# Kernel optimization log

Hardware: AMD Instinct MI355X
Metric: run time of the kernel (lower is better)

The kernel has to match this reference:

```python
import jax, jax.numpy as jnp
import numpy as np

B, N, D, H = 4, 2048, 512, 8
HD = D // H  # head_dim = 64
EPS = 1e-5


def setup_inputs() -> dict:
    key = jax.random.key(0)
    ks = jax.random.split(key, 12)
    x = jax.random.normal(ks[0], (B, N, D), dtype=jnp.float32)
    adj = jax.random.randint(ks[1], (B, N, N), 0, 2, dtype=jnp.int32)
    # self-loops so no softmax row is fully masked
    adj = jnp.maximum(adj, jnp.eye(N, dtype=jnp.int32)[None, :, :])
    s = 1.0 / np.sqrt(D)
    Wq = jax.random.uniform(ks[2], (D, D), jnp.float32, -s, s)
    bq = jnp.zeros((D,), jnp.float32)
    Wk = jax.random.uniform(ks[3], (D, D), jnp.float32, -s, s)
    bk = jnp.zeros((D,), jnp.float32)
    Wv = jax.random.uniform(ks[4], (D, D), jnp.float32, -s, s)
    bv = jnp.zeros((D,), jnp.float32)
    Wo = jax.random.uniform(ks[5], (D, D), jnp.float32, -s, s)
    bo = jnp.zeros((D,), jnp.float32)
    gamma = jnp.ones((D,), jnp.float32)
    beta = jnp.zeros((D,), jnp.float32)
    return {"x": x, "adj": adj, "Wq": Wq, "bq": bq, "Wk": Wk, "bk": bk,
            "Wv": Wv, "bv": bv, "Wo": Wo, "bo": bo, "gamma": gamma, "beta": beta}


def reference(x, adj, Wq, bq, Wk, bk, Wv, bv, Wo, bo, gamma, beta):
    b, n, d = x.shape
    scale = 1.0 / np.sqrt(HD).astype(np.float32)
    # QKV projections -> (b, n, H, HD)
    q = (x @ Wq + bq).reshape(b, n, H, HD)
    k = (x @ Wk + bk).reshape(b, n, H, HD)
    v = (x @ Wv + bv).reshape(b, n, H, HD)
    # scores: (b, H, n, n)
    scores = jnp.einsum('bnhd,bmhd->bhnm', q, k) * scale
    mask = (adj == 0)[:, None, :, :]  # (b, 1, n, n)
    scores = jnp.where(mask, jnp.float32(-jnp.inf), scores)
    attn = jax.nn.softmax(scores, axis=-1)
    h = jnp.einsum('bhnm,bmhd->bnhd', attn, v).reshape(b, n, d)
    h = h @ Wo + bo
    # residual + LayerNorm
    y = h + x
    mu = jnp.mean(y, axis=-1, keepdims=True)
    var = jnp.mean(jnp.square(y - mu), axis=-1, keepdims=True)
    return (y - mu) * jax.lax.rsqrt(var + EPS) * gamma + beta
```

## Files before the change

### kernel.cpp

```cpp
#include <hip/hip_runtime.h>
#include <hip/hip_bf16.h>

#define Bsz 4
#define Nn 2048
#define Dd 512
#define Hh 8
#define HDim 64
#define MTOT (Bsz * Nn)

typedef unsigned short ush;
typedef __bf16 bf16x8 __attribute__((ext_vector_type(8)));
typedef float f32x4 __attribute__((ext_vector_type(4)));

__device__ __forceinline__ ush f2bf(float f) {
    unsigned u = __builtin_bit_cast(unsigned, f);
    unsigned r = (u + 0x7fffu + ((u >> 16) & 1u)) >> 16;
    return (ush)r;
}
__device__ __forceinline__ unsigned cvtpk(float a, float b) {
    unsigned r;
    asm("v_cvt_pk_bf16_f32 %0, %1, %2" : "=v"(r) : "v"(a), "v"(b));
    return r;
}

#define GLOAD_LDS(g, l)                                                       \
    __builtin_amdgcn_global_load_lds(                                         \
        (const __attribute__((address_space(1))) unsigned int*)(g),           \
        (__attribute__((address_space(3))) unsigned int*)(l), 16, 0, 0)

__global__ __launch_bounds__(256) void convert_bf16(const float* __restrict__ src,
                                                    ush* __restrict__ dst, int n) {
    int i = (blockIdx.x * 256 + threadIdx.x) * 4;
    if (i < n) {
        float4 v = *reinterpret_cast<const float4*>(src + i);
        dst[i + 0] = f2bf(v.x);
        dst[i + 1] = f2bf(v.y);
        dst[i + 2] = f2bf(v.z);
        dst[i + 3] = f2bf(v.w);
    }
}

__global__ __launch_bounds__(256) void transpose_bf16(const float* __restrict__ src,
                                                      ush* __restrict__ dst) {
    __shared__ ush tile[64][72];
    const int k0 = blockIdx.x * 64, n0 = blockIdx.y * 64;
    const int t = threadIdx.x;
    const int r = t >> 2, c = (t & 3) * 16;
#pragma unroll
    for (int i = 0; i < 4; ++i) {
        float4 v = *reinterpret_cast<const float4*>(src + (size_t)(k0 + r) * Dd + n0 + c + i * 4);
        tile[r][c + i * 4 + 0] = f2bf(v.x);
        tile[r][c + i * 4 + 1] = f2bf(v.y);
        tile[r][c + i * 4 + 2] = f2bf(v.z);
        tile[r][c + i * 4 + 3] = f2bf(v.w);
    }
    __syncthreads();
    const int rn = t >> 2, kc = (t & 3) * 16;
    ush ov[16];
#pragma unroll
    for (int j = 0; j < 16; ++j) ov[j] = tile[kc + j][rn];
    *reinterpret_cast<uint4*>(dst + (size_t)(n0 + rn) * Dd + k0 + kc) =
        *reinterpret_cast<uint4*>(&ov[0]);
    *reinterpret_cast<uint4*>(dst + (size_t)(n0 + rn) * Dd + k0 + kc + 8) =
        *reinterpret_cast<uint4*>(&ov[8]);
}

__global__ __launch_bounds__(256) void adj_to_bits(const int* __restrict__ adj,
                                                   unsigned* __restrict__ bits) {
    int idx = blockIdx.x * 256 + threadIdx.x;
    const int* p = adj + (size_t)(idx >> 6) * Nn + (idx & 63) * 32;
    unsigned m = 0;
#pragma unroll
    for (int v4 = 0; v4 < 8; ++v4) {
        int4 v = *reinterpret_cast<const int4*>(p + v4 * 4);
        if (v.x) m |= 1u << (v4 * 4 + 0);
        if (v.y) m |= 1u << (v4 * 4 + 1);
        if (v.z) m |= 1u << (v4 * 4 + 2);
        if (v.w) m |= 1u << (v4 * 4 + 3);
    }
    bits[idx] = m;
}

__global__ __launch_bounds__(256) void gemm_bf16(const ush* __restrict__ A,
                                                 const ush* __restrict__ Wt,
                                                 const float* __restrict__ bias,
                                                 int mode, ush* __restrict__ outb,
                                                 float* __restrict__ outf) {
    __shared__ __align__(16) ush As[2][128][32];
    __shared__ __align__(16) ush Bs[2][64][32];
    const int t = threadIdx.x, lane = t & 63, w = t >> 6;
    const int ln = lane & 15, gr = lane >> 4;
    const int m0 = blockIdx.x * 128, n0 = blockIdx.y * 64;
    const int wm = w >> 1, wn = w & 1;

    f32x4 acc[4][2] = {};

    const int arow_in_op = lane >> 2;
    const int achk = (lane & 3) * 8;

#define STAGE_A(buf, k0)                                                          \
    {                                                                             \
        _Pragma("unroll") for (int o = 0; o < 2; ++o) {                           \
            int r0 = o * 64 + w * 16;                                             \
            int rr = r0 + arow_in_op;                                             \
            GLOAD_LDS(A + (size_t)(m0 + rr) * Dd + (k0) + achk, &As[buf][r0][0]); \
        }                                                                         \
    }
#define STAGE_B(buf, k0)                                                          \
    {                                                                             \
        int r0 = w * 16;                                                          \
        int rr = r0 + arow_in_op;                                                 \
        GLOAD_LDS(Wt + (size_t)(n0 + rr) * Dd + (k0) + achk, &Bs[buf][r0][0]);    \
    }

    STAGE_A(0, 0);
    STAGE_B(0, 0);
    __syncthreads();

    for (int it = 0; it < 16; ++it) {
        const int buf = it & 1;
        if (it < 15) {
            STAGE_A(buf ^ 1, (it + 1) * 32);
            STAGE_B(buf ^ 1, (it + 1) * 32);
        }
        bf16x8 af[4], bfr[2];
#pragma unroll
        for (int i = 0; i < 4; ++i)
            af[i] = *reinterpret_cast<const bf16x8*>(&As[buf][wm * 64 + i * 16 + ln][gr * 8]);
#pragma unroll
        for (int j = 0; j < 2; ++j)
            bfr[j] = *reinterpret_cast<const bf16x8*>(&Bs[buf][wn * 32 + j * 16 + ln][gr * 8]);
#pragma unroll
        for (int i = 0; i < 4; ++i)
#pragma unroll
            for (int j = 0; j < 2; ++j)
                acc[i][j] = __builtin_amdgcn_mfma_f32_16x16x32_bf16(af[i], bfr[j], acc[i][j], 0, 0, 0);
        __syncthreads();
    }

#pragma unroll
    for (int i = 0; i < 4; ++i) {
#pragma unroll
        for (int j = 0; j < 2; ++j) {
#pragma unroll
            for (int r = 0; r < 4; ++r) {
                int row = m0 + wm * 64 + i * 16 + gr * 4 + r;
                int col = n0 + wn * 32 + j * 16 + ln;
                float v = acc[i][j][r] + bias[col];
                if (mode == 2) {
                    outf[(size_t)row * Dd + col] = v;
                } else {
                    int b = row >> 11, n = row & (Nn - 1);
                    int h = col >> 6, hd = col & 63;
                    if (mode == 0)
                        outb[(((size_t)(b * Hh + h)) * Nn + n) * HDim + hd] = f2bf(v);
                    else
                        outb[(((size_t)(b * Hh + h)) * HDim + hd) * Nn + n] = f2bf(v);
                }
            }
        }
    }
#undef STAGE_A
#undef STAGE_B
}

__global__ __launch_bounds__(256) void attn_kernel(const ush* __restrict__ Q,
                                                   const ush* __restrict__ K,
                                                   const ush* __restrict__ Vt,
                                                   const unsigned* __restrict__ bits,
                                                   ush* __restrict__ O) {
    __shared__ __align__(16) ush Ktile[2][64][64];
    __shared__ __align__(16) ush Vtile[2][64][64];
    __shared__ __align__(16) ush Pl[4][16][64];
    const int t = threadIdx.x, lane = t & 63, w = t >> 6;
    const int ln = lane & 15, gr = lane >> 4;
    const int blk = blockIdx.x;
    const int qt = blk & 31;
    const int bh = blk >> 5;
    const int b = bh >> 3, h = bh & 7;
    const int q0 = qt * 64 + w * 16;

    const ush* Qb = Q + (size_t)bh * Nn * HDim;
    const ush* Kb = K + (size_t)bh * Nn * HDim;
    const ush* Vb = Vt + (size_t)bh * HDim * Nn;
    const unsigned* rowbits = bits + ((size_t)b * Nn + q0 + ln) * (Nn / 32);

    char* plbase = (char*)&Pl[w][0][0];
    const int lnm = ln & 7;

    const int srow_in_op = lane >> 3;
    const int schk = lane & 7;

#define STAGE_K(buf, kv0)                                                              \
    {                                                                                  \
        _Pragma("unroll") for (int o = 0; o < 2; ++o) {                                \
            int r0 = o * 32 + w * 8;                                                   \
            int rr = r0 + srow_in_op;                                                  \
            int cc = schk ^ (rr & 7);                                                  \
            GLOAD_LDS(Kb + (size_t)((kv0) + rr) * HDim + cc * 8, &Ktile[buf][r0][0]);  \
        }                                                                              \
    }
#define STAGE_V(buf, kv0)                                                              \
    {                                                                                  \
        _Pragma("unroll") for (int o = 0; o < 2; ++o) {                                \
            int r0 = o * 32 + w * 8;                                                   \
            int rr = r0 + srow_in_op;                                                  \
            int cc = schk ^ (rr & 7);                                                  \
            GLOAD_LDS(Vb + (size_t)rr * Nn + (kv0) + cc * 8, &Vtile[buf][r0][0]);      \
        }                                                                              \
    }

    bf16x8 bq0 = *reinterpret_cast<const bf16x8*>(Qb + (size_t)(q0 + ln) * HDim + gr * 8);
    bf16x8 bq1 = *reinterpret_cast<const bf16x8*>(Qb + (size_t)(q0 + ln) * HDim + 32 + gr * 8);

    f32x4 accO[4] = {};
    float mrow = -1e30f, lrow = 0.f;
    const float SCL = 0.125f * 1.44269504f;

    STAGE_K(0, 0);
    STAGE_V(0, 0);
    __syncthreads();

    for (int step = 0; step < 32; ++step) {
        const int kv0 = step * 64;
        const int buf = step & 1;
        if (step < 31) {
            STAGE_K(buf ^ 1, kv0 + 64);
            STAGE_V(buf ^ 1, kv0 + 64);
        }

        unsigned w0 = rowbits[kv0 >> 5];
        unsigned w1 = rowbits[(kv0 >> 5) + 1];

        f32x4 s[4];
#pragma unroll
        for (int kt = 0; kt < 4; ++kt) {
            bf16x8 a0 = *reinterpret_cast<const bf16x8*>(
                &Ktile[buf][kt * 16 + ln][((gr) ^ lnm) * 8]);
            bf16x8 a1 = *reinterpret_cast<const bf16x8*>(
                &Ktile[buf][kt * 16 + ln][((4 + gr) ^ lnm) * 8]);
            f32x4 z = {};
            z = __builtin_amdgcn_mfma_f32_16x16x32_bf16(a0, bq0, z, 0, 0, 0);
            s[kt] = __builtin_amdgcn_mfma_f32_16x16x32_bf16(a1, bq1, z, 0, 0, 0);
        }

        float p[4][4];
        float mk[4];
#pragma unroll
        for (int kt = 0; kt < 4; ++kt) {
            unsigned wsel = (kt >= 2) ? w1 : w0;
#pragma unroll
            for (int r = 0; r < 4; ++r) {
                float sv = s[kt][r] * SCL;
                int bit = (kt * 16 + 4 * gr + r) & 31;
                p[kt][r] = ((wsel >> bit) & 1u) ? sv : -1e30f;
            }
            mk[kt] = fmaxf(fmaxf(p[kt][0], p[kt][1]), fmaxf(p[kt][2], p[kt][3]));
        }
        float mc = fmaxf(fmaxf(mk[0], mk[1]), fmaxf(mk[2], mk[3]));
        mc = fmaxf(mc, __shfl_xor(mc, 16));
        mc = fmaxf(mc, __shfl_xor(mc, 32));
        float mn = fmaxf(mrow, mc);
        float alpha = __builtin_amdgcn_exp2f(mrow - mn);
        mrow = mn;

        float sk[4];
#pragma unroll
        for (int kt = 0; kt < 4; ++kt) {
#pragma unroll
            for (int r = 0; r < 4; ++r) p[kt][r] = __builtin_amdgcn_exp2f(p[kt][r] - mn);
            sk[kt] = (p[kt][0] + p[kt][1]) + (p[kt][2] + p[kt][3]);
        }
        float ps = (sk[0] + sk[1]) + (sk[2] + sk[3]);
        ps += __shfl_xor(ps, 16);
        ps += __shfl_xor(ps, 32);
        lrow = lrow * alpha + ps;
#pragma unroll
        for (int t2 = 0; t2 < 4; ++t2)
#pragma unroll
            for (int r = 0; r < 4; ++r) accO[t2][r] *= alpha;

#pragma unroll
        for (int kt = 0; kt < 4; ++kt) {
            unsigned pk0 = cvtpk(p[kt][0], p[kt][1]);
            unsigned pk1 = cvtpk(p[kt][2], p[kt][3]);
            int blkw = (2 * kt + (gr >> 1)) ^ lnm;
            *reinterpret_cast<uint2*>(plbase + ln * 128 + blkw * 16 + 8 * (gr & 1)) =
                make_uint2(pk0, pk1);
        }
#pragma unroll
        for (int c = 0; c < 2; ++c) {
            bf16x8 pf = *reinterpret_cast<const bf16x8*>(
                plbase + ln * 128 + (((4 * c + gr) ^ lnm) * 16));
#pragma unroll
            for (int t2 = 0; t2 < 4; ++t2) {
                bf16x8 vf = *reinterpret_cast<const bf16x8*>(
                    &Vtile[buf][t2 * 16 + ln][((c * 4 + gr) ^ lnm) * 8]);
                accO[t2] = __builtin_amdgcn_mfma_f32_16x16x32_bf16(vf, pf, accO[t2], 0, 0, 0);
            }
        }
        __syncthreads();
    }

    float inv = 1.0f / lrow;
#pragma unroll
    for (int t2 = 0; t2 < 4; ++t2) {
        unsigned o0 = cvtpk(accO[t2][0] * inv, accO[t2][1] * inv);
        unsigned o1 = cvtpk(accO[t2][2] * inv, accO[t2][3] * inv);
        int blkw = (2 * t2 + (gr >> 1)) ^ lnm;
        *reinterpret_cast<uint2*>(plbase + ln * 128 + blkw * 16 + 8 * (gr & 1)) =
            make_uint2(o0, o1);
    }
    int qr = lane >> 2, cs = lane & 3;
#pragma unroll
    for (int half = 0; half < 2; ++half) {
        int blkr = (cs * 2 + half) ^ (qr & 7);
        uint4 val = *reinterpret_cast<const uint4*>(plbase + qr * 128 + blkr * 16);
        *reinterpret_cast<uint4*>(O + ((size_t)(b * Nn + qt * 64 + w * 16 + qr)) * Dd +
                                  h * 64 + cs * 16 + half * 8) = val;
    }
#undef STAGE_K
#undef STAGE_V
}

__global__ __launch_bounds__(256) void ln_kernel(const float* __restrict__ hbuf,
                                                 const float* __restrict__ x,
                                                 const float* __restrict__ gamma,
                                                 const float* __restrict__ beta,
                                                 float* __restrict__ out) {
    const int row = blockIdx.x;
    const int t = threadIdx.x;
    const float* hr = hbuf + (size_t)row * Dd;
    const float* xr = x + (size_t)row * Dd;
    float y0 = hr[t] + xr[t];
    float y1 = hr[t + 256] + xr[t + 256];

    __shared__ float red[4];
    float s = y0 + y1;
#pragma unroll
    for (int m = 32; m; m >>= 1) s += __shfl_xor(s, m);
    if ((t & 63) == 0) red[t >> 6] = s;
    __syncthreads();
    float mu = (red[0] + red[1] + red[2] + red[3]) * (1.0f / Dd);

    float d0 = y0 - mu, d1 = y1 - mu;
    float vs = d0 * d0 + d1 * d1;
#pragma unroll
    for (int m = 32; m; m >>= 1) vs += __shfl_xor(vs, m);
    __syncthreads();
    if ((t & 63) == 0) red[t >> 6] = vs;
    __syncthreads();
    float var = (red[0] + red[1] + red[2] + red[3]) * (1.0f / Dd);
    float rs = rsqrtf(var + 1e-5f);

    out[(size_t)row * Dd + t] = d0 * rs * gamma[t] + beta[t];
    out[(size_t)row * Dd + t + 256] = d1 * rs * gamma[t + 256] + beta[t + 256];
}

extern "C" void kernel_launch(void* const* d_in, const int* in_sizes, int n_in,
                              void* d_out, int out_size, void* d_ws, size_t ws_size,
                              hipStream_t stream) {
    const float* x = (const float*)d_in[0];
    const int* adj = (const int*)d_in[1];
    const float* Wq = (const float*)d_in[2];
    const float* bq = (const float*)d_in[3];
    const float* Wk = (const float*)d_in[4];
    const float* bk = (const float*)d_in[5];
    const float* Wv = (const float*)d_in[6];
    const float* bv = (const float*)d_in[7];
    const float* Wo = (const float*)d_in[8];
    const float* bo = (const float*)d_in[9];
    const float* gamma = (const float*)d_in[10];
    const float* beta = (const float*)d_in[11];
    float* out = (float*)d_out;

    const size_t MD = (size_t)MTOT * Dd;
    const size_t WW = (size_t)Dd * Dd;
    ush* ws = (ush*)d_ws;
    ush* xb = ws;
    ush* Wqb = xb + MD;
    ush* Wkb = Wqb + WW;
    ush* Wvb = Wkb + WW;
    ush* Wob = Wvb + WW;
    ush* Qb = Wob + WW;
    ush* Kb = Qb + MD;
    ush* Vtb = Kb + MD;
    ush* Ob = Vtb + MD;
    float* hbuf = (float*)(Ob + MD);
    unsigned* bitsbuf = (unsigned*)hbuf;

    convert_bf16<<<dim3((int)(MD / 1024)), dim3(256), 0, stream>>>(x, xb, (int)MD);
    dim3 tg(Dd / 64, Dd / 64), bb(256);
    transpose_bf16<<<tg, bb, 0, stream>>>(Wq, Wqb);
    transpose_bf16<<<tg, bb, 0, stream>>>(Wk, Wkb);
    transpose_bf16<<<tg, bb, 0, stream>>>(Wv, Wvb);
    transpose_bf16<<<tg, bb, 0, stream>>>(Wo, Wob);

    adj_to_bits<<<dim3(MTOT * 64 / 256), dim3(256), 0, stream>>>(adj, bitsbuf);

    dim3 gg(MTOT / 128, Dd / 64);
    gemm_bf16<<<gg, bb, 0, stream>>>(xb, Wqb, bq, 0, Qb, nullptr);
    gemm_bf16<<<gg, bb, 0, stream>>>(xb, Wkb, bk, 0, Kb, nullptr);
    gemm_bf16<<<gg, bb, 0, stream>>>(xb, Wvb, bv, 1, Vtb, nullptr);

    attn_kernel<<<dim3(Bsz * Hh * (Nn / 64)), bb, 0, stream>>>(Qb, Kb, Vtb, bitsbuf, Ob);

    gemm_bf16<<<gg, bb, 0, stream>>>(Ob, Wob, bo, 2, nullptr, hbuf);

    ln_kernel<<<dim3(MTOT), bb, 0, stream>>>(hbuf, x, gamma, beta, out);
}
```

Before: 291.4 us.

## Fuse QKV projections into one 128x128 GEMM, fold scale, lazy softmax rescale

The three QKV projection GEMMs become a single launch over a concatenated transposed weight buffer, and the GEMM tile grows from 128x64 to 128x128 for more reuse per staged load. The softmax scale is folded into the Q projection epilogue, which removes a multiply per score in the attention loop. The attention kernel now skips the running-max update and the accumulator rescale unless the max grows by more than 8 in log2 units, cutting per-step VALU work. The risks are fewer blocks for the output projection, higher register pressure from the larger accumulator, and exp2 values up to 2^8 in bf16 P, which costs some precision headroom.

```diff
diff --git a/kernel.cpp b/kernel.cpp
--- a/kernel.cpp
+++ b/kernel.cpp
@@ -81,87 +81,96 @@
     bits[idx] = m;
 }
 
-__global__ __launch_bounds__(256) void gemm_bf16(const ush* __restrict__ A,
-                                                 const ush* __restrict__ Wt,
-                                                 const float* __restrict__ bias,
-                                                 int mode, ush* __restrict__ outb,
-                                                 float* __restrict__ outf) {
+__global__ __launch_bounds__(256) void gemm128(const ush* __restrict__ A,
+                                               const ush* __restrict__ Wt,
+                                               const float* __restrict__ bq,
+                                               const float* __restrict__ bk,
+                                               const float* __restrict__ bv,
+                                               ush* __restrict__ outQ,
+                                               ush* __restrict__ outK,
+                                               ush* __restrict__ outVt,
+                                               float* __restrict__ outF, int fused) {
     __shared__ __align__(16) ush As[2][128][32];
-    __shared__ __align__(16) ush Bs[2][64][32];
+    __shared__ __align__(16) ush Bs[2][128][32];
     const int t = threadIdx.x, lane = t & 63, w = t >> 6;
     const int ln = lane & 15, gr = lane >> 4;
-    const int m0 = blockIdx.x * 128, n0 = blockIdx.y * 64;
+    const int m0 = blockIdx.x * 128, n0 = blockIdx.y * 128;
     const int wm = w >> 1, wn = w & 1;
 
-    f32x4 acc[4][2] = {};
-
-    const int arow_in_op = lane >> 2;
-    const int achk = (lane & 3) * 8;
-
-#define STAGE_A(buf, k0)                                                          \
-    {                                                                             \
-        _Pragma("unroll") for (int o = 0; o < 2; ++o) {                           \
-            int r0 = o * 64 + w * 16;                                             \
-            int rr = r0 + arow_in_op;                                             \
-            GLOAD_LDS(A + (size_t)(m0 + rr) * Dd + (k0) + achk, &As[buf][r0][0]); \
-        }                                                                         \
-    }
-#define STAGE_B(buf, k0)                                                          \
-    {                                                                             \
-        int r0 = w * 16;                                                          \
-        int rr = r0 + arow_in_op;                                                 \
-        GLOAD_LDS(Wt + (size_t)(n0 + rr) * Dd + (k0) + achk, &Bs[buf][r0][0]);    \
-    }
-
-    STAGE_A(0, 0);
-    STAGE_B(0, 0);
+    f32x4 acc[4][4] = {};
+    const int srow = lane >> 2, schk = (lane & 3) * 8;
+
+#define STG(buf, k0)                                                               \
+    {                                                                              \
+        _Pragma("unroll") for (int o = 0; o < 2; ++o) {                            \
+            int r0 = o * 64 + w * 16;                                              \
+            int rr = r0 + srow;                                                    \
+            GLOAD_LDS(A + (size_t)(m0 + rr) * Dd + (k0) + schk, &As[buf][r0][0]);  \
+            GLOAD_LDS(Wt + (size_t)(n0 + rr) * Dd + (k0) + schk, &Bs[buf][r0][0]); \
+        }                                                                          \
+    }
+
+    STG(0, 0);
     __syncthreads();
 
     for (int it = 0; it < 16; ++it) {
         const int buf = it & 1;
-        if (it < 15) {
-            STAGE_A(buf ^ 1, (it + 1) * 32);
-            STAGE_B(buf ^ 1, (it + 1) * 32);
-        }
-        bf16x8 af[4], bfr[2];
+        if (it < 15) STG(buf ^ 1, (it + 1) * 32);
+        bf16x8 af[4], bf_[4];
 #pragma unroll
         for (int i = 0; i < 4; ++i)
             af[i] = *reinterpret_cast<const bf16x8*>(&As[buf][wm * 64 + i * 16 + ln][gr * 8]);
 #pragma unroll
-        for (int j = 0; j < 2; ++j)
-            bfr[j] = *reinterpret_cast<const bf16x8*>(&Bs[buf][wn * 32 + j * 16 + ln][gr * 8]);
+        for (int j = 0; j < 4; ++j)
+            bf_[j] = *reinterpret_cast<const bf16x8*>(&Bs[buf][wn * 64 + j * 16 + ln][gr * 8]);
 #pragma unroll
         for (int i = 0; i < 4; ++i)
 #pragma unroll
-            for (int j = 0; j < 2; ++j)
-                acc[i][j] = __builtin_amdgcn_mfma_f32_16x16x32_bf16(af[i], bfr[j], acc[i][j], 0, 0, 0);
+            for (int j = 0; j < 4; ++j)
+                acc[i][j] = __builtin_amdgcn_mfma_f32_16x16x32_bf16(af[i], bf_[j], acc[i][j], 0, 0, 0);
         __syncthreads();
     }
 
-#pragma unroll
-    for (int i = 0; i < 4; ++i) {
-#pragma unroll
-        for (int j = 0; j < 2; ++j) {
-#pragma unroll
-            for (int r = 0; r < 4; ++r) {
-                int row = m0 + wm * 64 + i * 16 + gr * 4 + r;
-                int col = n0 + wn * 32 + j * 16 + ln;
-                float v = acc[i][j][r] + bias[col];
-                if (mode == 2) {
-                    outf[(size_t)row * Dd + col] = v;
-                } else {
+    const float SCL = 0.125f * 1.44269504f;
+    if (fused) {
+        const int qkv = blockIdx.y >> 2;
+        const float* bias = (qkv == 0) ? bq : ((qkv == 1) ? bk : bv);
+        const float scale = (qkv == 0) ? SCL : 1.0f;
+#pragma unroll
+        for (int i = 0; i < 4; ++i) {
+#pragma unroll
+            for (int j = 0; j < 4; ++j) {
+#pragma unroll
+                for (int r = 0; r < 4; ++r) {
+                    int row = m0 + wm * 64 + i * 16 + gr * 4 + r;
+                    int colq = (n0 & 511) + wn * 64 + j * 16 + ln;
+                    float v = (acc[i][j][r] + bias[colq]) * scale;
                     int b = row >> 11, n = row & (Nn - 1);
-                    int h = col >> 6, hd = col & 63;
-                    if (mode == 0)
-                        outb[(((size_t)(b * Hh + h)) * Nn + n) * HDim + hd] = f2bf(v);
-                    else
-                        outb[(((size_t)(b * Hh + h)) * HDim + hd) * Nn + n] = f2bf(v);
+                    int h = colq >> 6, hd = colq & 63;
+                    if (qkv == 2)
+                        outVt[(((size_t)(b * Hh + h)) * HDim + hd) * Nn + n] = f2bf(v);
+                    else {
+                        ush* o = (qkv == 0) ? outQ : outK;
+                        o[(((size_t)(b * Hh + h)) * Nn + n) * HDim + hd] = f2bf(v);
+                    }
                 }
             }
         }
-    }
-#undef STAGE_A
-#undef STAGE_B
+    } else {
+#pragma unroll
+        for (int i = 0; i < 4; ++i) {
+#pragma unroll
+            for (int j = 0; j < 4; ++j) {
+#pragma unroll
+                for (int r = 0; r < 4; ++r) {
+                    int row = m0 + wm * 64 + i * 16 + gr * 4 + r;
+                    int col = n0 + wn * 64 + j * 16 + ln;
+                    outF[(size_t)row * Dd + col] = acc[i][j][r] + bq[col];
+                }
+            }
+        }
+    }
+#undef STG
 }
 
 __global__ __launch_bounds__(256) void attn_kernel(const ush* __restrict__ Q,
@@ -215,7 +224,6 @@
 
     f32x4 accO[4] = {};
     float mrow = -1e30f, lrow = 0.f;
-    const float SCL = 0.125f * 1.44269504f;
 
     STAGE_K(0, 0);
     STAGE_V(0, 0);
@@ -251,7 +259,7 @@
             unsigned wsel = (kt >= 2) ? w1 : w0;
 #pragma unroll
             for (int r = 0; r < 4; ++r) {
-                float sv = s[kt][r] * SCL;
+                float sv = s[kt][r];
                 int bit = (kt * 16 + 4 * gr + r) & 31;
                 p[kt][r] = ((wsel >> bit) & 1u) ? sv : -1e30f;
             }
@@ -260,25 +268,29 @@
         float mc = fmaxf(fmaxf(mk[0], mk[1]), fmaxf(mk[2], mk[3]));
         mc = fmaxf(mc, __shfl_xor(mc, 16));
         mc = fmaxf(mc, __shfl_xor(mc, 32));
-        float mn = fmaxf(mrow, mc);
-        float alpha = __builtin_amdgcn_exp2f(mrow - mn);
-        mrow = mn;
+
+        if (!__all(mc - mrow <= 8.0f)) {
+            float mn = fmaxf(mrow, mc);
+            float alpha = __builtin_amdgcn_exp2f(mrow - mn);
+            mrow = mn;
+            lrow *= alpha;
+#pragma unroll
+            for (int t2 = 0; t2 < 4; ++t2)
+#pragma unroll
+                for (int r = 0; r < 4; ++r) accO[t2][r] *= alpha;
+        }
 
         float sk[4];
 #pragma unroll
         for (int kt = 0; kt < 4; ++kt) {
 #pragma unroll
-            for (int r = 0; r < 4; ++r) p[kt][r] = __builtin_amdgcn_exp2f(p[kt][r] - mn);
+            for (int r = 0; r < 4; ++r) p[kt][r] = __builtin_amdgcn_exp2f(p[kt][r] - mrow);
             sk[kt] = (p[kt][0] + p[kt][1]) + (p[kt][2] + p[kt][3]);
         }
         float ps = (sk[0] + sk[1]) + (sk[2] + sk[3]);
         ps += __shfl_xor(ps, 16);
         ps += __shfl_xor(ps, 32);
-        lrow = lrow * alpha + ps;
-#pragma unroll
-        for (int t2 = 0; t2 < 4; ++t2)
-#pragma unroll
-            for (int r = 0; r < 4; ++r) accO[t2][r] *= alpha;
+        lrow += ps;
 
 #pragma unroll
         for (int kt = 0; kt < 4; ++kt) {
@@ -378,10 +390,8 @@
     const size_t WW = (size_t)Dd * Dd;
     ush* ws = (ush*)d_ws;
     ush* xb = ws;
-    ush* Wqb = xb + MD;
-    ush* Wkb = Wqb + WW;
-    ush* Wvb = Wkb + WW;
-    ush* Wob = Wvb + WW;
+    ush* Wqkvb = xb + MD;
+    ush* Wob = Wqkvb + 3 * WW;
     ush* Qb = Wob + WW;
     ush* Kb = Qb + MD;
     ush* Vtb = Kb + MD;
@@ -391,21 +401,20 @@
 
     convert_bf16<<<dim3((int)(MD / 1024)), dim3(256), 0, stream>>>(x, xb, (int)MD);
     dim3 tg(Dd / 64, Dd / 64), bb(256);
-    transpose_bf16<<<tg, bb, 0, stream>>>(Wq, Wqb);
-    transpose_bf16<<<tg, bb, 0, stream>>>(Wk, Wkb);
-    transpose_bf16<<<tg, bb, 0, stream>>>(Wv, Wvb);
+    transpose_bf16<<<tg, bb, 0, stream>>>(Wq, Wqkvb);
+    transpose_bf16<<<tg, bb, 0, stream>>>(Wk, Wqkvb + WW);
+    transpose_bf16<<<tg, bb, 0, stream>>>(Wv, Wqkvb + 2 * WW);
     transpose_bf16<<<tg, bb, 0, stream>>>(Wo, Wob);
 
     adj_to_bits<<<dim3(MTOT * 64 / 256), dim3(256), 0, stream>>>(adj, bitsbuf);
 
-    dim3 gg(MTOT / 128, Dd / 64);
-    gemm_bf16<<<gg, bb, 0, stream>>>(xb, Wqb, bq, 0, Qb, nullptr);
-    gemm_bf16<<<gg, bb, 0, stream>>>(xb, Wkb, bk, 0, Kb, nullptr);
-    gemm_bf16<<<gg, bb, 0, stream>>>(xb, Wvb, bv, 1, Vtb, nullptr);
+    gemm128<<<dim3(MTOT / 128, 12), bb, 0, stream>>>(xb, Wqkvb, bq, bk, bv,
+                                                     Qb, Kb, Vtb, nullptr, 1);
 
     attn_kernel<<<dim3(Bsz * Hh * (Nn / 64)), bb, 0, stream>>>(Qb, Kb, Vtb, bitsbuf, Ob);
 
-    gemm_bf16<<<gg, bb, 0, stream>>>(Ob, Wob, bo, 2, nullptr, hbuf);
+    gemm128<<<dim3(MTOT / 128, 4), bb, 0, stream>>>(Ob, Wob, bo, nullptr, nullptr,
+                                                    nullptr, nullptr, nullptr, hbuf, 0);
 
     ln_kernel<<<dim3(MTOT), bb, 0, stream>>>(hbuf, x, gamma, beta, out);
 }
```

Result: no change. 289.7 us (-0.6%).
